# Kernel optimization log

Measured on AMD Instinct MI355X. Metric: run time of the kernel, lower is better.

The kernel has to match this reference:

```python
import jax, jax.numpy as jnp
import numpy as np

B, T, M, VM = 64, 512, 8, 50  # batch, time, num_modules, rois per module
EPS = 1e-5  # BatchNorm eps


def setup_inputs() -> dict:
    key = jax.random.key(0)
    ks = jax.random.split(key, 12)
    x = jax.random.normal(ks[0], (B, M * VM, T, 1), jnp.float32)
    # learned adjacency, torch init = ones/V; perturb slightly
    PA = jnp.full((M, VM, VM), 1.0 / VM, jnp.float32) + 0.01 * jax.random.normal(ks[1], (M, VM, VM), jnp.float32)
    conv_w = jax.random.normal(ks[2], (M,), jnp.float32)          # 1x1 conv weight (1->1 chan) per module
    conv_b = 0.1 * jax.random.normal(ks[3], (M,), jnp.float32)
    bn_gamma = 1.0 + 0.1 * jax.random.normal(ks[4], (M,), jnp.float32)
    bn_beta = 0.1 * jax.random.normal(ks[5], (M,), jnp.float32)
    bn_mean = 0.1 * jax.random.normal(ks[6], (M,), jnp.float32)
    bn_var = jax.random.uniform(ks[7], (M,), jnp.float32) + 0.5   # positive
    w1 = jax.random.normal(ks[8], (M, 8), jnp.float32) * 0.5      # Linear(1,8) weight per module
    b1 = 0.1 * jax.random.normal(ks[9], (M, 8), jnp.float32)
    w2 = jax.random.normal(ks[10], (M, 8), jnp.float32) * 0.5     # Linear(8,1) weight per module
    b2 = 0.1 * jax.random.normal(ks[11], (M,), jnp.float32)
    return dict(x=x, PA=PA, conv_w=conv_w, conv_b=conv_b, bn_gamma=bn_gamma, bn_beta=bn_beta,
                bn_mean=bn_mean, bn_var=bn_var, w1=w1, b1=b1, w2=w2, b2=b2)


def reference(x, PA, conv_w, conv_b, bn_gamma, bn_beta, bn_mean, bn_var, w1, b1, w2, b2):
    # x: [B, V_total, T, 1]; torch permute(0,3,2,1) -> [B, C=1, T, V_total]
    xp = x[..., 0].transpose(0, 2, 1)                 # [B, T, V_total]
    xm = xp.reshape(B, T, M, VM)                      # contiguous module blocks == index_select
    # UnitGCN: x_agg = x @ A per module
    agg = jnp.einsum('btmv,mvw->btmw', xm, PA)        # [B, T, M, VM]
    # 1x1 conv (scalar per module) + BatchNorm2d(1) in eval mode + ReLU
    y = agg * conv_w[:, None] + conv_b[:, None]
    scale = bn_gamma / jnp.sqrt(bn_var + EPS)
    h = jax.nn.relu((y - bn_mean[:, None]) * scale[:, None] + bn_beta[:, None])
    # AttentionPooling: MLP(1->8->1) on channel dim, softmax over nodes, weighted sum
    hid = jnp.tanh(h[..., None] * w1[:, None, :] + b1[:, None, :])   # [B, T, M, VM, 8]
    score = jnp.einsum('btmvh,mh->btmv', hid, w2) + b2[:, None]      # [B, T, M, VM]
    attn = jax.nn.softmax(score, axis=3)
    pooled = jnp.sum(h * attn, axis=3)                # [B, T, M]
    # concat over modules on dim 1 -> [B, M, T, 1]
    return pooled.transpose(0, 2, 1)[..., None]
```

## Files before the change

kernel.cpp:

```cpp
#include <hip/hip_runtime.h>

#define BB 64
#define TT 512
#define MM 8
#define VMM 50
#define TBLK 128
#define RSTRIDE 36
#define EPSV 1e-5f

#define TN   1024
#define HMAX 16.0f
#define HSTEP (HMAX / TN)
#define INVH  (TN / HMAX)

using short8  = __attribute__((ext_vector_type(8))) short;
using float4v = __attribute__((ext_vector_type(4))) float;

__device__ __forceinline__ float fast_rcp(float x) {
    return __builtin_amdgcn_rcpf(x);
}
__device__ __forceinline__ float fast_tanh(float x) {
    float e2 = __expf(2.0f * x);
    return fmaf(-2.0f, fast_rcp(e2 + 1.0f), 1.0f);
}
__device__ __forceinline__ unsigned f2bf(float f) {
    unsigned u = __float_as_uint(f);
    return (u + 0x7FFFu + ((u >> 16) & 1u)) >> 16;
}
__device__ __forceinline__ unsigned pack2(float lo, float hi) {
    return f2bf(lo) | (f2bf(hi) << 16);
}
__device__ __forceinline__ unsigned packh2(float lo, float hi) {
    unsigned short a = __builtin_bit_cast(unsigned short, (_Float16)lo);
    unsigned short b = __builtin_bit_cast(unsigned short, (_Float16)hi);
    return (unsigned)a | ((unsigned)b << 16);
}
__device__ __forceinline__ float h2f_lo(unsigned p) {
    return (float)__builtin_bit_cast(_Float16, (unsigned short)(p & 0xFFFFu));
}
__device__ __forceinline__ float h2f_hi(unsigned p) {
    return (float)__builtin_bit_cast(_Float16, (unsigned short)(p >> 16));
}

__global__ __launch_bounds__(256, 4)
void intra_module_agg_kernel(const float* __restrict__ x,
                             const float* __restrict__ PA,
                             const float* __restrict__ conv_w,
                             const float* __restrict__ conv_b,
                             const float* __restrict__ bn_gamma,
                             const float* __restrict__ bn_beta,
                             const float* __restrict__ bn_mean,
                             const float* __restrict__ bn_var,
                             const float* __restrict__ w1,
                             const float* __restrict__ b1,
                             const float* __restrict__ w2,
                             const float* __restrict__ b2,
                             float* __restrict__ out)
{
    const int blk = blockIdx.x;
    const int tq  = blk & 3;
    const int m   = (blk >> 2) & 7;
    const int b   = blk >> 5;
    const int j   = threadIdx.x;

    __shared__ __align__(16) unsigned xsu[TBLK * RSTRIDE];
    __shared__ __align__(16) unsigned psu[64 * RSTRIDE];
    __shared__ unsigned gt[TN];

    const float scale = bn_gamma[m] * __frsqrt_rn(bn_var[m] + EPSV);
    const float Amul  = conv_w[m] * scale;
    const float Cadd  = (conv_b[m] - bn_mean[m]) * scale + bn_beta[m];

    {
        const int t  = j >> 1;
        const int hf = j & 1;
        const float* xb = x + ((b * (MM * VMM) + m * VMM) * TT + tq * TBLK + t);
        unsigned* row = &xsu[t * RSTRIDE];
        const int vp0 = hf * 13;
#pragma unroll
        for (int i = 0; i < 13; ++i) {
            int vp = vp0 + i;
            float a = 0.0f, c = 0.0f;
            if (vp < 25) { a = xb[(2 * vp) * TT]; c = xb[(2 * vp + 1) * TT]; }
            row[vp] = pack2(a, c);
        }
        if (hf) {
#pragma unroll
            for (int vp = 26; vp < 32; ++vp) row[vp] = 0u;
        }
    }

    {
        const float* pa = PA + m * (VMM * VMM);
        const int w  = j & 63;
        const int vb = (j >> 6) * 8;
#pragma unroll
        for (int i = 0; i < 8; ++i) {
            int vp = vb + i, v0 = 2 * vp, v1 = v0 + 1;
            float a = (w < VMM && v0 < VMM) ? pa[v0 * VMM + w] : 0.0f;
            float c = (w < VMM && v1 < VMM) ? pa[v1 * VMM + w] : 0.0f;
            psu[w * RSTRIDE + vp] = pack2(a, c);
        }
    }

    {
        float W1[8], B1[8], W2[8];
        float B2 = b2[m], sabs = 0.0f;
#pragma unroll
        for (int k = 0; k < 8; ++k) {
            W1[k] = w1[m * 8 + k];
            B1[k] = b1[m * 8 + k];
            W2[k] = w2[m * 8 + k];
            sabs += fabsf(W2[k]);
        }
        const float s0 = (B2 + sabs) - 8.0f;
        float gv[5];
#pragma unroll
        for (int k = 0; k < 5; ++k) {
            float h = (4 * j + k) * HSTEP;
            float s = B2 - s0;
#pragma unroll
            for (int i = 0; i < 8; ++i)
                s = fmaf(W2[i], fast_tanh(fmaf(h, W1[i], B1[i])), s);
            gv[k] = __expf(s);
        }
#pragma unroll
        for (int k = 0; k < 4; ++k)
            gt[4 * j + k] = packh2(gv[k], gv[k + 1] - gv[k]);
    }

    __syncthreads();

    const int lane = j & 63, wv = j >> 6;
    const int q = lane >> 4, nl = lane & 15;

    short8 A[4][2];
#pragma unroll
    for (int wt = 0; wt < 4; ++wt)
#pragma unroll
        for (int ks = 0; ks < 2; ++ks)
            A[wt][ks] = *(const short8*)&psu[(wt * 16 + nl) * RSTRIDE + ks * 16 + q * 4];

    float4v C[2][4];
#pragma unroll
    for (int t2 = 0; t2 < 2; ++t2)
#pragma unroll
        for (int wt = 0; wt < 4; ++wt)
            C[t2][wt] = (float4v){0.f, 0.f, 0.f, 0.f};

#pragma unroll
    for (int t2 = 0; t2 < 2; ++t2) {
        const int trow = (wv * 2 + t2) * 16 + nl;
        short8 Bv0 = *(const short8*)&xsu[trow * RSTRIDE + 0 * 16 + q * 4];
        short8 Bv1 = *(const short8*)&xsu[trow * RSTRIDE + 1 * 16 + q * 4];
#pragma unroll
        for (int wt = 0; wt < 4; ++wt) {
            C[t2][wt] = __builtin_amdgcn_mfma_f32_16x16x32_bf16(A[wt][0], Bv0, C[t2][wt], 0, 0, 0);
            C[t2][wt] = __builtin_amdgcn_mfma_f32_16x16x32_bf16(A[wt][1], Bv1, C[t2][wt], 0, 0, 0);
        }
    }

    const int obase = (b * MM + m) * TT + tq * TBLK;
#pragma unroll
    for (int t2 = 0; t2 < 2; ++t2) {
        float se = 0.0f, sh = 0.0f;
#pragma unroll
        for (int wt = 0; wt < 4; ++wt) {
#pragma unroll
            for (int r = 0; r < 4; ++r) {
                const int w = wt * 16 + q * 4 + r;
                float h = fmaxf(fmaf(C[t2][wt][r], Amul, Cadd), 0.0f);
                float u = fminf(h, HMAX - 0.0005f) * INVH;
                int   i = (int)u;
                float fr = u - (float)i;
                unsigned p = gt[i];
                float e = (w < VMM) ? fmaf(fr, h2f_hi(p), h2f_lo(p)) : 0.0f;
                se += e;
                sh = fmaf(h, e, sh);
            }
        }
        se += __shfl_xor(se, 16, 64);
        se += __shfl_xor(se, 32, 64);
        sh += __shfl_xor(sh, 16, 64);
        sh += __shfl_xor(sh, 32, 64);
        if (q == 0)
            out[obase + (wv * 2 + t2) * 16 + nl] = sh * fast_rcp(se);
    }
}

extern "C" void kernel_launch(void* const* d_in, const int* in_sizes, int n_in,
                              void* d_out, int out_size, void* d_ws, size_t ws_size,
                              hipStream_t stream) {
    const float* x        = (const float*)d_in[0];
    const float* PA       = (const float*)d_in[1];
    const float* conv_w   = (const float*)d_in[2];
    const float* conv_b   = (const float*)d_in[3];
    const float* bn_gamma = (const float*)d_in[4];
    const float* bn_beta  = (const float*)d_in[5];
    const float* bn_mean  = (const float*)d_in[6];
    const float* bn_var   = (const float*)d_in[7];
    const float* w1       = (const float*)d_in[8];
    const float* b1       = (const float*)d_in[9];
    const float* w2       = (const float*)d_in[10];
    const float* b2       = (const float*)d_in[11];
    float* out = (float*)d_out;

    dim3 grid(BB * MM * (TT / TBLK));
    dim3 block(256);
    intra_module_agg_kernel<<<grid, block, 0, stream>>>(
        x, PA, conv_w, conv_b, bn_gamma, bn_beta, bn_mean, bn_var,
        w1, b1, w2, b2, out);
}
```

Baseline: 113.6 us.

## Precompute per-module exp lookup table and packed PA in a prep kernel

A small prep kernel now builds, once per module, the tanh-MLP exp lookup table and the bf16-packed adjacency matrix in workspace memory. Each main block then copies them into LDS with vector loads instead of recomputing 40 tanh and 5 exp per thread and gathering PA. This removes redundant transcendental work repeated across 2048 blocks, at the cost of an extra kernel launch and a serial dependency between the two kernels. If the workspace is too small, the original single kernel is used as a fallback.

After: 112.5 us. About the same (-1.0%).

```diff
diff --git a/kernel.cpp b/kernel.cpp
--- a/kernel.cpp
+++ b/kernel.cpp
@@ -13,6 +13,10 @@
 #define HSTEP (HMAX / TN)
 #define INVH  (TN / HMAX)
 
+#define WS_GT(m)  ((m) * TN)
+#define WS_PA(m)  (MM * TN + (m) * (64 * 32))
+#define WS_NEED   ((MM * TN + MM * 64 * 32) * 4)
+
 using short8  = __attribute__((ext_vector_type(8))) short;
 using float4v = __attribute__((ext_vector_type(4))) float;
 
@@ -43,18 +47,65 @@
 }
 
 __global__ __launch_bounds__(256, 4)
+void prep_kernel(const float* __restrict__ PA,
+                 const float* __restrict__ w1,
+                 const float* __restrict__ b1,
+                 const float* __restrict__ w2,
+                 const float* __restrict__ b2,
+                 unsigned* __restrict__ ws)
+{
+    const int m = blockIdx.x;
+    const int j = threadIdx.x;
+
+    {
+        float W1[8], B1[8], W2[8];
+        float B2 = b2[m], sabs = 0.0f;
+#pragma unroll
+        for (int k = 0; k < 8; ++k) {
+            W1[k] = w1[m * 8 + k];
+            B1[k] = b1[m * 8 + k];
+            W2[k] = w2[m * 8 + k];
+            sabs += fabsf(W2[k]);
+        }
+        const float s0 = (B2 + sabs) - 8.0f;
+        float gv[5];
+#pragma unroll
+        for (int k = 0; k < 5; ++k) {
+            float h = (4 * j + k) * HSTEP;
+            float s = B2 - s0;
+#pragma unroll
+            for (int i = 0; i < 8; ++i)
+                s = fmaf(W2[i], fast_tanh(fmaf(h, W1[i], B1[i])), s);
+            gv[k] = __expf(s);
+        }
+#pragma unroll
+        for (int k = 0; k < 4; ++k)
+            ws[WS_GT(m) + 4 * j + k] = packh2(gv[k], gv[k + 1] - gv[k]);
+    }
+
+    {
+        const float* pa = PA + m * (VMM * VMM);
+        const int w  = j & 63;
+        const int vb = (j >> 6) * 8;
+#pragma unroll
+        for (int i = 0; i < 8; ++i) {
+            int vp = vb + i, v0 = 2 * vp, v1 = v0 + 1;
+            float a = (w < VMM && v0 < VMM) ? pa[v0 * VMM + w] : 0.0f;
+            float c = (w < VMM && v1 < VMM) ? pa[v1 * VMM + w] : 0.0f;
+            ws[WS_PA(m) + w * 32 + vp] = pack2(a, c);
+        }
+    }
+}
+
+__global__ __launch_bounds__(256, 4)
 void intra_module_agg_kernel(const float* __restrict__ x,
-                             const float* __restrict__ PA,
                              const float* __restrict__ conv_w,
                              const float* __restrict__ conv_b,
                              const float* __restrict__ bn_gamma,
                              const float* __restrict__ bn_beta,
                              const float* __restrict__ bn_mean,
                              const float* __restrict__ bn_var,
-                             const float* __restrict__ w1,
-                             const float* __restrict__ b1,
-                             const float* __restrict__ w2,
-                             const float* __restrict__ b2,
+                             const unsigned* __restrict__ ws,
                              float* __restrict__ out)
 {
     const int blk = blockIdx.x;
@@ -65,11 +116,27 @@
 
     __shared__ __align__(16) unsigned xsu[TBLK * RSTRIDE];
     __shared__ __align__(16) unsigned psu[64 * RSTRIDE];
-    __shared__ unsigned gt[TN];
+    __shared__ __align__(16) unsigned gt[TN];
 
     const float scale = bn_gamma[m] * __frsqrt_rn(bn_var[m] + EPSV);
     const float Amul  = conv_w[m] * scale;
     const float Cadd  = (conv_b[m] - bn_mean[m]) * scale + bn_beta[m];
+
+    {
+        uint4 g = ((const uint4*)(ws + WS_GT(m)))[j];
+        *(uint4*)&gt[4 * j] = g;
+    }
+    {
+        const uint4* src = (const uint4*)(ws + WS_PA(m));
+#pragma unroll
+        for (int p = 0; p < 2; ++p) {
+            int i4 = j + p * 256;
+            uint4 v = src[i4];
+            int r = i4 >> 3;
+            int c = (i4 & 7) * 4;
+            *(uint4*)&psu[r * RSTRIDE + c] = v;
+        }
+    }
 
     {
         const int t  = j >> 1;
@@ -90,6 +157,112 @@
         }
     }
 
+    __syncthreads();
+
+    const int lane = j & 63, wv = j >> 6;
+    const int q = lane >> 4, nl = lane & 15;
+
+    short8 A[4][2];
+#pragma unroll
+    for (int wt = 0; wt < 4; ++wt)
+#pragma unroll
+        for (int ks = 0; ks < 2; ++ks)
+            A[wt][ks] = *(const short8*)&psu[(wt * 16 + nl) * RSTRIDE + ks * 16 + q * 4];
+
+    float4v C[2][4];
+#pragma unroll
+    for (int t2 = 0; t2 < 2; ++t2)
+#pragma unroll
+        for (int wt = 0; wt < 4; ++wt)
+            C[t2][wt] = (float4v){0.f, 0.f, 0.f, 0.f};
+
+#pragma unroll
+    for (int t2 = 0; t2 < 2; ++t2) {
+        const int trow = (wv * 2 + t2) * 16 + nl;
+        short8 Bv0 = *(const short8*)&xsu[trow * RSTRIDE + 0 * 16 + q * 4];
+        short8 Bv1 = *(const short8*)&xsu[trow * RSTRIDE + 1 * 16 + q * 4];
+#pragma unroll
+        for (int wt = 0; wt < 4; ++wt) {
+            C[t2][wt] = __builtin_amdgcn_mfma_f32_16x16x32_bf16(A[wt][0], Bv0, C[t2][wt], 0, 0, 0);
+            C[t2][wt] = __builtin_amdgcn_mfma_f32_16x16x32_bf16(A[wt][1], Bv1, C[t2][wt], 0, 0, 0);
+        }
+    }
+
+    const int obase = (b * MM + m) * TT + tq * TBLK;
+#pragma unroll
+    for (int t2 = 0; t2 < 2; ++t2) {
+        float se = 0.0f, sh = 0.0f;
+#pragma unroll
+        for (int wt = 0; wt < 4; ++wt) {
+#pragma unroll
+            for (int r = 0; r < 4; ++r) {
+                const int w = wt * 16 + q * 4 + r;
+                float h = fmaxf(fmaf(C[t2][wt][r], Amul, Cadd), 0.0f);
+                float u = fminf(h, HMAX - 0.0005f) * INVH;
+                int   i = (int)u;
+                float fr = u - (float)i;
+                unsigned p = gt[i];
+                float e = (w < VMM) ? fmaf(fr, h2f_hi(p), h2f_lo(p)) : 0.0f;
+                se += e;
+                sh = fmaf(h, e, sh);
+            }
+        }
+        se += __shfl_xor(se, 16, 64);
+        se += __shfl_xor(se, 32, 64);
+        sh += __shfl_xor(sh, 16, 64);
+        sh += __shfl_xor(sh, 32, 64);
+        if (q == 0)
+            out[obase + (wv * 2 + t2) * 16 + nl] = sh * fast_rcp(se);
+    }
+}
+
+__global__ __launch_bounds__(256, 4)
+void mono_kernel(const float* __restrict__ x,
+                 const float* __restrict__ PA,
+                 const float* __restrict__ conv_w,
+                 const float* __restrict__ conv_b,
+                 const float* __restrict__ bn_gamma,
+                 const float* __restrict__ bn_beta,
+                 const float* __restrict__ bn_mean,
+                 const float* __restrict__ bn_var,
+                 const float* __restrict__ w1,
+                 const float* __restrict__ b1,
+                 const float* __restrict__ w2,
+                 const float* __restrict__ b2,
+                 float* __restrict__ out)
+{
+    const int blk = blockIdx.x;
+    const int tq  = blk & 3;
+    const int m   = (blk >> 2) & 7;
+    const int b   = blk >> 5;
+    const int j   = threadIdx.x;
+
+    __shared__ __align__(16) unsigned xsu[TBLK * RSTRIDE];
+    __shared__ __align__(16) unsigned psu[64 * RSTRIDE];
+    __shared__ __align__(16) unsigned gt[TN];
+
+    const float scale = bn_gamma[m] * __frsqrt_rn(bn_var[m] + EPSV);
+    const float Amul  = conv_w[m] * scale;
+    const float Cadd  = (conv_b[m] - bn_mean[m]) * scale + bn_beta[m];
+
+    {
+        const int t  = j >> 1;
+        const int hf = j & 1;
+        const float* xb = x + ((b * (MM * VMM) + m * VMM) * TT + tq * TBLK + t);
+        unsigned* row = &xsu[t * RSTRIDE];
+        const int vp0 = hf * 13;
+#pragma unroll
+        for (int i = 0; i < 13; ++i) {
+            int vp = vp0 + i;
+            float a = 0.0f, c = 0.0f;
+            if (vp < 25) { a = xb[(2 * vp) * TT]; c = xb[(2 * vp + 1) * TT]; }
+            row[vp] = pack2(a, c);
+        }
+        if (hf) {
+#pragma unroll
+            for (int vp = 26; vp < 32; ++vp) row[vp] = 0u;
+        }
+    }
     {
         const float* pa = PA + m * (VMM * VMM);
         const int w  = j & 63;
@@ -102,7 +275,6 @@
             psu[w * RSTRIDE + vp] = pack2(a, c);
         }
     }
-
     {
         float W1[8], B1[8], W2[8];
         float B2 = b2[m], sabs = 0.0f;
@@ -205,9 +377,14 @@
     const float* b2       = (const float*)d_in[11];
     float* out = (float*)d_out;
 
-    dim3 grid(BB * MM * (TT / TBLK));
-    dim3 block(256);
-    intra_module_agg_kernel<<<grid, block, 0, stream>>>(
-        x, PA, conv_w, conv_b, bn_gamma, bn_beta, bn_mean, bn_var,
-        w1, b1, w2, b2, out);
-}
+    if (ws_size >= (size_t)WS_NEED) {
+        unsigned* ws = (unsigned*)d_ws;
+        prep_kernel<<<dim3(MM), dim3(256), 0, stream>>>(PA, w1, b1, w2, b2, ws);
+        intra_module_agg_kernel<<<dim3(BB * MM * (TT / TBLK)), dim3(256), 0, stream>>>(
+            x, conv_w, conv_b, bn_gamma, bn_beta, bn_mean, bn_var, ws, out);
+    } else {
+        mono_kernel<<<dim3(BB * MM * (TT / TBLK)), dim3(256), 0, stream>>>(
+            x, PA, conv_w, conv_b, bn_gamma, bn_beta, bn_mean, bn_var,
+            w1, b1, w2, b2, out);
+    }
+}
```
